# Optimization experiments

Hardware: AMD Instinct MI355X
Metric: run time of the kernel (lower is better)

## Reference

```python
import jax, jax.numpy as jnp
import numpy as np

B, C, R, Cc = 16384, 30, 7, 7

def setup_inputs() -> dict:
    key = jax.random.key(0)
    k1, k2, k3 = jax.random.split(key, 3)
    pred = jax.random.uniform(k1, (B, C, R, Cc), dtype=jnp.float32)
    label = jax.random.uniform(k2, (B, C, R, Cc), dtype=jnp.float32)
    obj = (jax.random.uniform(k3, (B, R, Cc)) > 0.7).astype(jnp.float32)
    label = label.at[:, 4].set(obj)
    return {"pred": pred, "label": label}

def _boxes(t, cols, rows, nrow, ncol, off):
    # t: [b,30,r,c]; channels off..off+3 are (x,y,w,h) relative to cell
    x, y, w, h = t[:, off], t[:, off + 1], t[:, off + 2], t[:, off + 3]
    cx = (x + cols) / ncol
    cy = (y + rows) / nrow
    return cx - w / 2, cy - h / 2, cx + w / 2, cy + h / 2

def _iou(a, b):
    ax1, ay1, ax2, ay2 = a
    bx1, by1, bx2, by2 = b
    iw = jnp.maximum(jnp.minimum(ax2, bx2) - jnp.maximum(ax1, bx1), 0.0)
    ih = jnp.maximum(jnp.minimum(ay2, by2) - jnp.maximum(ay1, by1), 0.0)
    inter = iw * ih
    area_a = (ax2 - ax1) * (ay2 - ay1)
    area_b = (bx2 - bx1) * (by2 - by1)
    return inter / (area_a + area_b - inter + 1e-10)

def reference(pred, label):
    b_size = pred.shape[0]
    nrow, ncol = pred.shape[-2], pred.shape[-1]
    cols = jnp.arange(ncol, dtype=pred.dtype)[None, None, :]  # [1,1,c]
    rows = jnp.arange(nrow, dtype=pred.dtype)[None, :, None]  # [1,r,1]

    bbox1 = _boxes(pred, cols, rows, nrow, ncol, 0)
    bbox2 = _boxes(pred, cols, rows, nrow, ncol, 5)
    lbox = _boxes(label, cols, rows, nrow, ncol, 0)
    iou1 = _iou(bbox1, lbox)  # [b,r,c]
    iou2 = _iou(bbox2, lbox)
    choose1 = iou1 >= iou2

    # coord loss candidates (sum over the 2 xy channels / 2 wh channels)
    coord1 = 5.0 * jnp.sum((pred[:, 0:2] - label[:, 0:2]) ** 2, axis=1) \
           + jnp.sum((jnp.sqrt(pred[:, 2:4]) - jnp.sqrt(label[:, 2:4])) ** 2, axis=1)
    coord2 = 5.0 * jnp.sum((pred[:, 5:7] - label[:, 5:7]) ** 2, axis=1) \
           + jnp.sum((jnp.sqrt(pred[:, 7:9]) - jnp.sqrt(label[:, 7:9])) ** 2, axis=1)

    obj1 = (pred[:, 4] - iou1) ** 2
    obj2 = (pred[:, 9] - iou2) ** 2

    coord = jnp.where(choose1, coord1, coord2)
    obj_conf = jnp.where(choose1, obj1, obj2)
    noobj_conf_obj = 0.5 * jnp.where(choose1, obj2, obj1)
    class_l = jnp.sum((pred[:, 10:] - label[:, 10:]) ** 2, axis=1)

    obj_cell = coord + obj_conf + noobj_conf_obj + class_l
    # note: original sums the two confidences THEN squares (faithful to source)
    noobj_cell = 0.5 * (pred[:, 4] + pred[:, 9]) ** 2

    is_obj = label[:, 4] == 1.0
    per_cell = jnp.where(is_obj, obj_cell, noobj_cell)
    return jnp.sum(per_cell) / b_size
```

## Files before the change

### kernel.cpp

```cpp
#include <hip/hip_runtime.h>


#define NBATCH 16384
#define NCH 30
#define NCELL 49
#define BSTRIDE 1470
#define BLOCK 256
#define NB 2
#define CHUNK (NB * BSTRIDE)
#define CHUNK4 (CHUNK / 4)
#define NBLOCKS (NBATCH / NB)

__device__ __forceinline__ float sq(float x) { return x * x; }

__device__ __forceinline__ float iou_vs_label(float x, float y, float w, float h,
                                              float fc, float fr,
                                              float lx1, float ly1, float lx2, float ly2,
                                              float larea) {
    const float inv7 = 1.0f / 7.0f;
    float cx = (x + fc) * inv7;
    float cy = (y + fr) * inv7;
    float hw = w * 0.5f, hh = h * 0.5f;
    float x1 = cx - hw, y1 = cy - hh;
    float x2 = cx + hw, y2 = cy + hh;
    float iw = fmaxf(fminf(x2, lx2) - fmaxf(x1, lx1), 0.0f);
    float ih = fmaxf(fminf(y2, ly2) - fmaxf(y1, ly1), 0.0f);
    float inter = iw * ih;
    float area = (x2 - x1) * (y2 - y1);
    return inter / (area + larea - inter + 1e-10f);
}

__global__ __launch_bounds__(BLOCK) void yolo_loss_main(const float* __restrict__ pred,
                                                        const float* __restrict__ label,
                                                        float* __restrict__ partials) {
    __shared__ float4 sp4[CHUNK4];
    __shared__ float4 sl4[CHUNK4];

    const int blk = blockIdx.x;

    {
        const float4* gp = (const float4*)(pred + (size_t)blk * CHUNK);
        const float4* gl = (const float4*)(label + (size_t)blk * CHUNK);
#pragma unroll
        for (int it = 0; it < 3; ++it) {
            int i = it * BLOCK + threadIdx.x;
            if (i < CHUNK4) {
                sp4[i] = gp[i];
                sl4[i] = gl[i];
            }
        }
    }
    __syncthreads();

    float per_cell = 0.0f;
    if (threadIdx.x < NB * NCELL) {
        const int lb = threadIdx.x / NCELL;
        const int rc = threadIdx.x - lb * NCELL;
        const int r = rc / 7;
        const int c = rc - r * 7;

        const float* sp = (const float*)sp4 + lb * BSTRIDE + rc;
        const float* sl = (const float*)sl4 + lb * BSTRIDE + rc;

        float p[NCH], l[NCH];
#pragma unroll
        for (int ch = 0; ch < NCH; ++ch) {
            p[ch] = sp[ch * NCELL];
            l[ch] = sl[ch * NCELL];
        }

        const float fc = (float)c, fr = (float)r;
        const float inv7 = 1.0f / 7.0f;

        float lcx = (l[0] + fc) * inv7;
        float lcy = (l[1] + fr) * inv7;
        float lhw = l[2] * 0.5f, lhh = l[3] * 0.5f;
        float lx1 = lcx - lhw, ly1 = lcy - lhh;
        float lx2 = lcx + lhw, ly2 = lcy + lhh;
        float larea = (lx2 - lx1) * (ly2 - ly1);

        float iou1 = iou_vs_label(p[0], p[1], p[2], p[3], fc, fr, lx1, ly1, lx2, ly2, larea);
        float iou2 = iou_vs_label(p[5], p[6], p[7], p[8], fc, fr, lx1, ly1, lx2, ly2, larea);
        bool choose1 = iou1 >= iou2;

        float coord1 = 5.0f * (sq(p[0] - l[0]) + sq(p[1] - l[1]))
                     + sq(sqrtf(p[2]) - sqrtf(l[2])) + sq(sqrtf(p[3]) - sqrtf(l[3]));
        float coord2 = 5.0f * (sq(p[5] - l[5]) + sq(p[6] - l[6]))
                     + sq(sqrtf(p[7]) - sqrtf(l[7])) + sq(sqrtf(p[8]) - sqrtf(l[8]));

        float obj1 = sq(p[4] - iou1);
        float obj2 = sq(p[9] - iou2);

        float coord      = choose1 ? coord1 : coord2;
        float obj_conf   = choose1 ? obj1 : obj2;
        float noobj_conf = 0.5f * (choose1 ? obj2 : obj1);

        float class_l = 0.0f;
#pragma unroll
        for (int ch = 10; ch < NCH; ++ch) class_l += sq(p[ch] - l[ch]);

        float obj_cell = coord + obj_conf + noobj_conf + class_l;
        float psum = p[4] + p[9];
        float noobj_cell = 0.5f * psum * psum;

        per_cell = (l[4] == 1.0f) ? obj_cell : noobj_cell;
    }

    float v = per_cell;
#pragma unroll
    for (int off = 32; off > 0; off >>= 1) v += __shfl_down(v, off, 64);

    __shared__ float smem[BLOCK / 64];
    const int lane = threadIdx.x & 63;
    const int wave = threadIdx.x >> 6;
    if (lane == 0) smem[wave] = v;
    __syncthreads();
    if (threadIdx.x == 0) {
        partials[blk] = smem[0] + smem[1] + smem[2] + smem[3];
    }
}

__global__ __launch_bounds__(BLOCK) void yolo_loss_reduce(const float* __restrict__ partials,
                                                          float* __restrict__ out) {
    float s = 0.0f;
#pragma unroll
    for (int it = 0; it < NBLOCKS / BLOCK; ++it)
        s += partials[it * BLOCK + threadIdx.x];

#pragma unroll
    for (int off = 32; off > 0; off >>= 1) s += __shfl_down(s, off, 64);

    __shared__ float smem[BLOCK / 64];
    const int lane = threadIdx.x & 63;
    const int wave = threadIdx.x >> 6;
    if (lane == 0) smem[wave] = s;
    __syncthreads();
    if (threadIdx.x == 0) {
        out[0] = (smem[0] + smem[1] + smem[2] + smem[3]) * (1.0f / (float)NBATCH);
    }
}

extern "C" void kernel_launch(void* const* d_in, const int* in_sizes, int n_in,
                              void* d_out, int out_size, void* d_ws, size_t ws_size,
                              hipStream_t stream) {
    const float* pred  = (const float*)d_in[0];
    const float* label = (const float*)d_in[1];
    float* out = (float*)d_out;
    float* partials = (float*)d_ws;

    yolo_loss_main<<<NBLOCKS, BLOCK, 0, stream>>>(pred, label, partials);
    yolo_loss_reduce<<<1, BLOCK, 0, stream>>>(partials, out);
}
```

Before: 204.4 us.

## Use persistent blocks with double-buffered async global-to-LDS loads

Replaces the one-chunk-per-block launch with a fixed grid of 768 persistent blocks. Each block loops over chunks and prefetches the next chunk into a second LDS buffer with direct global_load_lds instructions while it computes on the current one. Each thread keeps a running sum across chunks, and the final reduce kernel reads fewer partials. This aims to overlap memory latency with compute and avoid staging data through registers. In exchange it doubles LDS use per block and relies on the barrier to wait for the async LDS writes.

```diff
diff --git a/kernel.cpp b/kernel.cpp
--- a/kernel.cpp
+++ b/kernel.cpp
@@ -9,7 +9,11 @@
 #define NB 2
 #define CHUNK (NB * BSTRIDE)
 #define CHUNK4 (CHUNK / 4)
-#define NBLOCKS (NBATCH / NB)
+#define NCHUNKS (NBATCH / NB)
+#define GRID 768
+
+typedef __attribute__((address_space(1))) const void gvoid;
+typedef __attribute__((address_space(3))) void lvoid;
 
 __device__ __forceinline__ float sq(float x) { return x * x; }
 
@@ -33,90 +37,105 @@
 __global__ __launch_bounds__(BLOCK) void yolo_loss_main(const float* __restrict__ pred,
                                                         const float* __restrict__ label,
                                                         float* __restrict__ partials) {
-    __shared__ float4 sp4[CHUNK4];
-    __shared__ float4 sl4[CHUNK4];
+    __shared__ float4 sp4[2][CHUNK4];
+    __shared__ float4 sl4[2][CHUNK4];
+    __shared__ float smem[BLOCK / 64];
 
-    const int blk = blockIdx.x;
+    const int tid = threadIdx.x;
 
-    {
-        const float4* gp = (const float4*)(pred + (size_t)blk * CHUNK);
-        const float4* gl = (const float4*)(label + (size_t)blk * CHUNK);
+    auto stage = [&](int c, int b) {
+        const float4* gp = (const float4*)(pred + (size_t)c * CHUNK);
+        const float4* gl = (const float4*)(label + (size_t)c * CHUNK);
 #pragma unroll
         for (int it = 0; it < 3; ++it) {
-            int i = it * BLOCK + threadIdx.x;
+            int i = it * BLOCK + tid;
             if (i < CHUNK4) {
-                sp4[i] = gp[i];
-                sl4[i] = gl[i];
+                __builtin_amdgcn_global_load_lds((gvoid*)(gp + i), (lvoid*)&sp4[b][i], 16, 0, 0);
+                __builtin_amdgcn_global_load_lds((gvoid*)(gl + i), (lvoid*)&sl4[b][i], 16, 0, 0);
             }
         }
-    }
+    };
+
+    const int lb = tid / NCELL;
+    const int rc = tid - lb * NCELL;
+    const int r = rc / 7;
+    const int c7 = rc - r * 7;
+    const float fc = (float)c7, fr = (float)r;
+    const float inv7 = 1.0f / 7.0f;
+    const bool active = tid < NB * NCELL;
+
+    float acc = 0.0f;
+
+    int c = blockIdx.x;
+    stage(c, 0);
     __syncthreads();
+    int buf = 0;
 
-    float per_cell = 0.0f;
-    if (threadIdx.x < NB * NCELL) {
-        const int lb = threadIdx.x / NCELL;
-        const int rc = threadIdx.x - lb * NCELL;
-        const int r = rc / 7;
-        const int c = rc - r * 7;
+    while (true) {
+        int nextc = c + GRID;
+        if (nextc < NCHUNKS) stage(nextc, buf ^ 1);
 
-        const float* sp = (const float*)sp4 + lb * BSTRIDE + rc;
-        const float* sl = (const float*)sl4 + lb * BSTRIDE + rc;
+        if (active) {
+            const float* sp = (const float*)&sp4[buf][0] + lb * BSTRIDE + rc;
+            const float* sl = (const float*)&sl4[buf][0] + lb * BSTRIDE + rc;
 
-        float p[NCH], l[NCH];
+            float p[NCH], l[NCH];
 #pragma unroll
-        for (int ch = 0; ch < NCH; ++ch) {
-            p[ch] = sp[ch * NCELL];
-            l[ch] = sl[ch * NCELL];
+            for (int ch = 0; ch < NCH; ++ch) {
+                p[ch] = sp[ch * NCELL];
+                l[ch] = sl[ch * NCELL];
+            }
+
+            float lcx = (l[0] + fc) * inv7;
+            float lcy = (l[1] + fr) * inv7;
+            float lhw = l[2] * 0.5f, lhh = l[3] * 0.5f;
+            float lx1 = lcx - lhw, ly1 = lcy - lhh;
+            float lx2 = lcx + lhw, ly2 = lcy + lhh;
+            float larea = (lx2 - lx1) * (ly2 - ly1);
+
+            float iou1 = iou_vs_label(p[0], p[1], p[2], p[3], fc, fr, lx1, ly1, lx2, ly2, larea);
+            float iou2 = iou_vs_label(p[5], p[6], p[7], p[8], fc, fr, lx1, ly1, lx2, ly2, larea);
+            bool choose1 = iou1 >= iou2;
+
+            float coord1 = 5.0f * (sq(p[0] - l[0]) + sq(p[1] - l[1]))
+                         + sq(sqrtf(p[2]) - sqrtf(l[2])) + sq(sqrtf(p[3]) - sqrtf(l[3]));
+            float coord2 = 5.0f * (sq(p[5] - l[5]) + sq(p[6] - l[6]))
+                         + sq(sqrtf(p[7]) - sqrtf(l[7])) + sq(sqrtf(p[8]) - sqrtf(l[8]));
+
+            float obj1 = sq(p[4] - iou1);
+            float obj2 = sq(p[9] - iou2);
+
+            float coord      = choose1 ? coord1 : coord2;
+            float obj_conf   = choose1 ? obj1 : obj2;
+            float noobj_conf = 0.5f * (choose1 ? obj2 : obj1);
+
+            float class_l = 0.0f;
+#pragma unroll
+            for (int ch = 10; ch < NCH; ++ch) class_l += sq(p[ch] - l[ch]);
+
+            float obj_cell = coord + obj_conf + noobj_conf + class_l;
+            float psum = p[4] + p[9];
+            float noobj_cell = 0.5f * psum * psum;
+
+            acc += (l[4] == 1.0f) ? obj_cell : noobj_cell;
         }
 
-        const float fc = (float)c, fr = (float)r;
-        const float inv7 = 1.0f / 7.0f;
-
-        float lcx = (l[0] + fc) * inv7;
-        float lcy = (l[1] + fr) * inv7;
-        float lhw = l[2] * 0.5f, lhh = l[3] * 0.5f;
-        float lx1 = lcx - lhw, ly1 = lcy - lhh;
-        float lx2 = lcx + lhw, ly2 = lcy + lhh;
-        float larea = (lx2 - lx1) * (ly2 - ly1);
-
-        float iou1 = iou_vs_label(p[0], p[1], p[2], p[3], fc, fr, lx1, ly1, lx2, ly2, larea);
-        float iou2 = iou_vs_label(p[5], p[6], p[7], p[8], fc, fr, lx1, ly1, lx2, ly2, larea);
-        bool choose1 = iou1 >= iou2;
-
-        float coord1 = 5.0f * (sq(p[0] - l[0]) + sq(p[1] - l[1]))
-                     + sq(sqrtf(p[2]) - sqrtf(l[2])) + sq(sqrtf(p[3]) - sqrtf(l[3]));
-        float coord2 = 5.0f * (sq(p[5] - l[5]) + sq(p[6] - l[6]))
-                     + sq(sqrtf(p[7]) - sqrtf(l[7])) + sq(sqrtf(p[8]) - sqrtf(l[8]));
-
-        float obj1 = sq(p[4] - iou1);
-        float obj2 = sq(p[9] - iou2);
-
-        float coord      = choose1 ? coord1 : coord2;
-        float obj_conf   = choose1 ? obj1 : obj2;
-        float noobj_conf = 0.5f * (choose1 ? obj2 : obj1);
-
-        float class_l = 0.0f;
-#pragma unroll
-        for (int ch = 10; ch < NCH; ++ch) class_l += sq(p[ch] - l[ch]);
-
-        float obj_cell = coord + obj_conf + noobj_conf + class_l;
-        float psum = p[4] + p[9];
-        float noobj_cell = 0.5f * psum * psum;
-
-        per_cell = (l[4] == 1.0f) ? obj_cell : noobj_cell;
+        __syncthreads();
+        if (nextc >= NCHUNKS) break;
+        c = nextc;
+        buf ^= 1;
     }
 
-    float v = per_cell;
+    float v = acc;
 #pragma unroll
     for (int off = 32; off > 0; off >>= 1) v += __shfl_down(v, off, 64);
 
-    __shared__ float smem[BLOCK / 64];
-    const int lane = threadIdx.x & 63;
-    const int wave = threadIdx.x >> 6;
+    const int lane = tid & 63;
+    const int wave = tid >> 6;
     if (lane == 0) smem[wave] = v;
     __syncthreads();
-    if (threadIdx.x == 0) {
-        partials[blk] = smem[0] + smem[1] + smem[2] + smem[3];
+    if (tid == 0) {
+        partials[blockIdx.x] = smem[0] + smem[1] + smem[2] + smem[3];
     }
 }
 
@@ -124,7 +143,7 @@
                                                           float* __restrict__ out) {
     float s = 0.0f;
 #pragma unroll
-    for (int it = 0; it < NBLOCKS / BLOCK; ++it)
+    for (int it = 0; it < GRID / BLOCK; ++it)
         s += partials[it * BLOCK + threadIdx.x];
 
 #pragma unroll
@@ -148,6 +167,6 @@
     float* out = (float*)d_out;
     float* partials = (float*)d_ws;
 
-    yolo_loss_main<<<NBLOCKS, BLOCK, 0, stream>>>(pred, label, partials);
+    yolo_loss_main<<<GRID, BLOCK, 0, stream>>>(pred, label, partials);
     yolo_loss_reduce<<<1, BLOCK, 0, stream>>>(partials, out);
 }
```

Result: no change. 205.2 us (+0.4%).
